# Kernel optimization log

Measured on AMD Instinct MI355X. Metric: run time of the kernel, lower is better.

Reference implementation:

```python
import jax, jax.numpy as jnp
import numpy as np
from jax import lax

B, T, V, E, H, L = 128, 256, 50000, 300, 512, 96


def masked_lstm(x, mask, W, U, b):
    """Keras-semantics masked LSTM, return_sequences=True.
    x: [B,T,D], mask: [B,T] bool. Gate order i,f,c,o (Keras).
    Masked steps carry h,c forward (output at masked step = previous output)."""
    Hs = U.shape[0]
    # input-to-hidden done as one big GEMM outside the scan
    xg = jnp.einsum('btd,dg->btg', x, W) + b  # [B,T,4H]
    h0 = jnp.zeros((x.shape[0], Hs), x.dtype)
    c0 = jnp.zeros((x.shape[0], Hs), x.dtype)

    def step(carry, inp):
        h, c = carry
        g_x, m = inp  # [B,4H], [B]
        g = g_x + h @ U
        i = jax.nn.sigmoid(g[:, :Hs])
        f = jax.nn.sigmoid(g[:, Hs:2 * Hs])
        cand = jnp.tanh(g[:, 2 * Hs:3 * Hs])
        o = jax.nn.sigmoid(g[:, 3 * Hs:])
        c_new = f * c + i * cand
        h_new = o * jnp.tanh(c_new)
        m = m[:, None]
        h_new = jnp.where(m, h_new, h)
        c_new = jnp.where(m, c_new, c)
        return (h_new, c_new), h_new

    (_, _), hs = lax.scan(step, (h0, c0), (xg.transpose(1, 0, 2), mask.T))
    return hs.transpose(1, 0, 2)  # [B,T,H]


def setup_inputs() -> dict:
    key = jax.random.key(0)
    ks = jax.random.split(key, 11)
    word_ids = jax.random.randint(ks[0], (B, T), 0, V, dtype=jnp.int32)
    predicate_ids = jax.random.randint(ks[1], (B, T), 0, 2, dtype=jnp.int32)
    emb = jax.random.normal(ks[2], (V, E), jnp.float32) * 0.1
    W1 = jax.random.normal(ks[3], (E + 1, 4 * H), jnp.float32) * 0.05
    U1 = jax.random.normal(ks[4], (H, 4 * H), jnp.float32) * 0.05
    b1 = jnp.zeros((4 * H,), jnp.float32)
    W2 = jax.random.normal(ks[5], (H, 4 * H), jnp.float32) * 0.05
    U2 = jax.random.normal(ks[6], (H, 4 * H), jnp.float32) * 0.05
    b2 = jnp.zeros((4 * H,), jnp.float32)
    Wd = jax.random.normal(ks[7], (H, L), jnp.float32) * 0.05
    bd = jnp.zeros((L,), jnp.float32)
    return {"word_ids": word_ids, "predicate_ids": predicate_ids,
            "emb": emb, "W1": W1, "U1": U1, "b1": b1,
            "W2": W2, "U2": U2, "b2": b2, "Wd": Wd, "bd": bd,
            "training": 0}


def reference(word_ids, predicate_ids, emb, W1, U1, b1, W2, U2, b2, Wd, bd, training):
    # training=0 -> dropout disabled (keep_prob=1.0 anyway)
    mask = word_ids != 0  # mask_zero semantics of the Embedding layer
    x = emb[word_ids]  # [B,T,E]
    flag = predicate_ids.astype(x.dtype)[..., None]  # [B,T,1]
    x = jnp.concatenate([x, flag], axis=2)  # [B,T,E+1]
    h1 = masked_lstm(x, mask, W1, U1, b1)
    h2 = masked_lstm(h1, mask, W2, U2, b2)
    enc = h2.reshape(-1, U1.shape[0])  # [B*T, H]
    return jax.nn.softmax(enc @ Wd + bd, axis=-1)  # [B*T, L]
```

## Files before the change

kernel.cpp:

```cpp
#include <hip/hip_runtime.h>
#include <hip/hip_bf16.h>

#define T_SEQ 256
#define HID 512
#define G4 2048
#define ASTR 80

typedef __attribute__((ext_vector_type(8))) short short8;
typedef __attribute__((ext_vector_type(4))) float floatx4;
typedef __attribute__((ext_vector_type(4))) int intx4;

__device__ inline unsigned short f2bf(float f) {
  union { __hip_bfloat16 h; unsigned short u; } cv;
  cv.h = __float2bfloat16(f);
  return cv.u;
}
__device__ inline float bf2f(unsigned short u) {
  union { unsigned short u; __hip_bfloat16 h; } cv;
  cv.u = u;
  return __bfloat162float(cv.h);
}
__device__ inline float fsigmoid(float x) {
  return __builtin_amdgcn_rcpf(1.0f + __expf(-x));
}
__device__ inline float ftanh(float x) {
  float e = __expf(2.0f * x);
  return 1.0f - 2.0f * __builtin_amdgcn_rcpf(e + 1.0f);
}

__device__ __forceinline__ void bar_lgkm() {
  asm volatile("s_waitcnt lgkmcnt(0)\n\ts_barrier" ::: "memory");
}

__global__ __launch_bounds__(256) void transpose_bf16(const float* __restrict__ src,
                                                      unsigned short* __restrict__ dst,
                                                      int K, int N, int Kpad) {
  __shared__ float tile[32][33];
  int n0 = blockIdx.x * 32, k0 = blockIdx.y * 32;
  int tx = threadIdx.x & 31, ty = threadIdx.x >> 5;
#pragma unroll
  for (int i = 0; i < 32; i += 8) {
    int k = k0 + ty + i, n = n0 + tx;
    tile[ty + i][tx] = (k < K) ? src[(size_t)k * N + n] : 0.0f;
  }
  __syncthreads();
#pragma unroll
  for (int i = 0; i < 32; i += 8) {
    int n = n0 + ty + i, k = k0 + tx;
    dst[(size_t)n * Kpad + k] = f2bf(tile[tx][ty + i]);
  }
}

__global__ __launch_bounds__(256) void gemm_xg1(const float* __restrict__ emb,
                                                const int* __restrict__ wid,
                                                const int* __restrict__ pred,
                                                const unsigned short* __restrict__ Bt,
                                                unsigned short* __restrict__ C) {
  int m0 = blockIdx.x * 64;
  int tid = threadIdx.x, lane = tid & 63, w = tid >> 6;
  __shared__ __align__(16) short As[64][328];
  __shared__ __align__(16) short Bs[2][64][40];
  {
    int grow = tid >> 2, gpart = tid & 3;
    int wrow = wid[m0 + grow];
    float pflag = (float)pred[m0 + grow];
    const float* erow = emb + (size_t)wrow * 300;
#pragma unroll
    for (int i = 0; i < 10; i++) {
      int c0 = gpart * 80 + i * 8;
      float f[8];
      if (c0 + 8 <= 300) {
        float4 x0 = *(const float4*)(erow + c0);
        float4 x1 = *(const float4*)(erow + c0 + 4);
        f[0] = x0.x; f[1] = x0.y; f[2] = x0.z; f[3] = x0.w;
        f[4] = x1.x; f[5] = x1.y; f[6] = x1.z; f[7] = x1.w;
      } else {
#pragma unroll
        for (int j = 0; j < 8; j++) {
          int k = c0 + j;
          f[j] = (k < 300) ? erow[k] : ((k == 300) ? pflag : 0.0f);
        }
      }
      short8 v;
#pragma unroll
      for (int j = 0; j < 8; j++) v[j] = (short)f2bf(f[j]);
      *(short8*)&As[grow][c0] = v;
    }
  }
  int brow = tid >> 2, bpart = tid & 3;
  for (int n0 = 0; n0 < 2048; n0 += 64) {
    *(short8*)&Bs[0][brow][bpart * 8] =
        *(const short8*)(Bt + (size_t)(n0 + brow) * 320 + bpart * 8);
    bar_lgkm();
    floatx4 acc[4];
#pragma unroll
    for (int i = 0; i < 4; i++) acc[i] = (floatx4){0.f, 0.f, 0.f, 0.f};
#pragma unroll
    for (int ks = 0; ks < 10; ks++) {
      if (ks < 9)
        *(short8*)&Bs[(ks + 1) & 1][brow][bpart * 8] =
            *(const short8*)(Bt + (size_t)(n0 + brow) * 320 + (ks + 1) * 32 + bpart * 8);
      short8 afr = *(const short8*)&As[w * 16 + (lane & 15)][ks * 32 + (lane >> 4) * 8];
#pragma unroll
      for (int nc = 0; nc < 4; nc++) {
        short8 bfr = *(const short8*)&Bs[ks & 1][nc * 16 + (lane & 15)][(lane >> 4) * 8];
        acc[nc] = __builtin_amdgcn_mfma_f32_16x16x32_bf16(afr, bfr, acc[nc], 0, 0, 0);
      }
      bar_lgkm();
    }
#pragma unroll
    for (int nc = 0; nc < 4; nc++)
#pragma unroll
      for (int r = 0; r < 4; r++) {
        int rr = m0 + w * 16 + ((lane >> 4) << 2) + r;
        int cc = n0 + nc * 16 + (lane & 15);
        C[(size_t)rr * G4 + cc] = f2bf(acc[nc][r]);
      }
  }
}

__device__ __forceinline__ void stage_issue(const unsigned int* base, int c16,
                                            intx4 (&v)[8], unsigned done) {
#pragma unroll
  for (int i = 0; i < 8; i++) {
    if (!(done & (1u << i))) {
      const unsigned int* p = base + 8 * c16 + 128 * (i >> 1) + 4 * (i & 1);
      asm volatile("global_load_dwordx4 %0, %1, off sc0 sc1" : "=v"(v[i]) : "v"(p) : "memory");
    }
  }
}
__device__ __forceinline__ void stage_check(unsigned want, char* AhRow, int sw, int c16,
                                            intx4 (&v)[8], unsigned& done) {
  asm volatile("s_waitcnt vmcnt(0)" ::: "memory");
#pragma unroll
  for (int i = 0; i < 8; i++) {
    if (!(done & (1u << i))) {
      intx4 a = v[i];
      unsigned u0 = (unsigned)a.x, u1 = (unsigned)a.y, u2 = (unsigned)a.z, u3 = (unsigned)a.w;
      bool ok = ((u0 >> 16) == want) & ((u1 >> 16) == want) & ((u2 >> 16) == want) &
                ((u3 >> 16) == want);
      if (ok) {
        unsigned lo = (u0 & 0xffffu) | (u1 << 16);
        unsigned hi = (u2 & 0xffffu) | (u3 << 16);
        int s = c16 + 16 * (i >> 1);
        uint2 pp; pp.x = lo; pp.y = hi;
        *(uint2*)(AhRow + ((s * 16) ^ sw) + (i & 1) * 8) = pp;
        done |= (1u << i);
      }
    }
  }
}
__device__ __forceinline__ void stage_wait(const unsigned int* base, unsigned want,
                                           char* AhRow, int sw, int c16) {
  intx4 v[8];
  unsigned done = 0;
  stage_issue(base, c16, v, done);
  stage_check(want, AhRow, sw, c16, v, done);
  while (done != 0xFFu) {
    __builtin_amdgcn_s_sleep(1);
    stage_issue(base, c16, v, done);
    stage_check(want, AhRow, sw, c16, v, done);
  }
}

__global__ __launch_bounds__(256, 1) void lstm_merged(
    const unsigned short* __restrict__ xg1,
    const unsigned short* __restrict__ Ut1, const float* __restrict__ b1,
    const unsigned short* __restrict__ Wt2, const unsigned short* __restrict__ Ut2,
    const float* __restrict__ b2, const int* __restrict__ wid,
    unsigned int* ex, unsigned short* h2seq) {
  const int blk = blockIdx.x;
  const int bgrp = blk & 7, jblk = blk >> 3;
  const int b0 = bgrp * 16, j0 = jblk * 16;
  const int tid = threadIdx.x, lane = tid & 63, w = tid >> 6;

  __shared__ __align__(16) char AhA[16 * 1024];
  __shared__ __align__(16) char AhB[16 * 1024];
  __shared__ float g1s[4][16][16];
  __shared__ float g2s[4][16][16];
  __shared__ float cst1[16][16];
  __shared__ float cst2[16][16];
  __shared__ __align__(16) unsigned short xgt[4][16][16];

  const int row = tid >> 4, c16 = tid & 15;
  const int sw = (row & 7) << 4;
  char* AhRowA = AhA + row * 1024;
  char* AhRowB = AhB + row * 1024;
  const int ucol = w * 512 + j0 + (lane & 15);
  const int* widp = wid + (size_t)(b0 + row) * T_SEQ;

  short8 uf1[16], wf2[16], uf2[16];
  {
    const unsigned short* p1 = Ut1 + (size_t)ucol * 512 + ((lane >> 4) * 8);
    const unsigned short* p2 = Wt2 + (size_t)ucol * 512 + ((lane >> 4) * 8);
    const unsigned short* p3 = Ut2 + (size_t)ucol * 512 + ((lane >> 4) * 8);
#pragma unroll
    for (int kk = 0; kk < 16; kk++) {
      uf1[kk] = *(const short8*)(p1 + kk * 32);
      wf2[kk] = *(const short8*)(p2 + kk * 32);
      uf2[kk] = *(const short8*)(p3 + kk * 32);
    }
  }
  float b1v = b1[ucol], b2v = b2[ucol];
  cst1[row][c16] = 0.0f;
  cst2[row][c16] = 0.0f;
  {
    short8 z = {0, 0, 0, 0, 0, 0, 0, 0};
    for (int i = tid; i < 1024; i += 256) {
      *(short8*)(AhA + i * 16) = z;
      *(short8*)(AhB + i * 16) = z;
    }
  }
  __syncthreads();

  int xg_g = tid >> 6, xg_rw = (tid >> 2) & 15, xg_part = tid & 3;
  uint2 xpf = *(const uint2*)(xg1 + ((size_t)(b0 + xg_rw) * T_SEQ + 0) * G4 + xg_g * 512 + j0 +
                              xg_part * 4);
  int mcur = widp[0];
  int mprev = 0;

  const size_t SLOT = (size_t)2 * 128 * 512;
  const int frow = lane & 15, kbase = (lane >> 4) * 16, fsw = (frow & 7) << 4;

  for (int t = 0; t <= T_SEQ; t++) {
    if (t > 0) {
      const unsigned int* bA = ex + (size_t)((t - 1) & 1) * SLOT + (size_t)(b0 + row) * 512;
      stage_wait(bA, (unsigned)t, AhRowA, sw, c16);
    }
    if (t < T_SEQ) {
      *(uint2*)(&xgt[xg_g][xg_rw][xg_part * 4]) = xpf;
      if (t + 1 < T_SEQ)
        xpf = *(const uint2*)(xg1 + ((size_t)(b0 + xg_rw) * T_SEQ + (t + 1)) * G4 + xg_g * 512 +
                              j0 + xg_part * 4);
    }
    bar_lgkm();

    floatx4 a1x = (floatx4){0.f, 0.f, 0.f, 0.f};
    floatx4 a1y = (floatx4){0.f, 0.f, 0.f, 0.f};
#pragma unroll
    for (int kk = 0; kk < 16; kk += 2) {
      short8 a0 = *(const short8*)(AhA + frow * 1024 + ((kk * 64 + kbase) ^ fsw));
      short8 a1 = *(const short8*)(AhA + frow * 1024 + (((kk + 1) * 64 + kbase) ^ fsw));
      a1x = __builtin_amdgcn_mfma_f32_16x16x32_bf16(a0, uf1[kk], a1x, 0, 0, 0);
      a1y = __builtin_amdgcn_mfma_f32_16x16x32_bf16(a1, uf1[kk + 1], a1y, 0, 0, 0);
    }
    if (t < T_SEQ) {
#pragma unroll
      for (int r = 0; r < 4; r++) {
        int grow = ((lane >> 4) << 2) + r, gcol = lane & 15;
        g1s[w][grow][gcol] = a1x[r] + a1y[r] + b1v + bf2f(xgt[w][grow][gcol]);
      }
    }
    bar_lgkm();

    if (t < T_SEQ) {
      float gi = g1s[0][row][c16], gf = g1s[1][row][c16];
      float gc = g1s[2][row][c16], go = g1s[3][row][c16];
      float iv = fsigmoid(gi), fv = fsigmoid(gf), cd = ftanh(gc), ov = fsigmoid(go);
      float cold = cst1[row][c16];
      float cn = fv * cold + iv * cd;
      float hn = ov * ftanh(cn);
      if (mcur == 0) {
        cn = cold;
        hn = bf2f(*(const unsigned short*)(AhRowA + (((j0 + c16) * 2) ^ sw)));
      }
      cst1[row][c16] = cn;
      unsigned v1 = (((unsigned)(t + 1)) << 16) | f2bf(hn);
      unsigned int* d1 = ex + (size_t)(t & 1) * SLOT + (size_t)(b0 + row) * 512 + j0 + c16;
      asm volatile("global_store_dword %0, %1, off sc0 sc1" ::"v"(d1), "v"(v1) : "memory");
    }
    if (t == 0) {
      unsigned v2 = 1u << 16;
      unsigned int* d2 =
          ex + (size_t)128 * 512 + (size_t)(b0 + row) * 512 + j0 + c16;
      asm volatile("global_store_dword %0, %1, off sc0 sc1" ::"v"(d2), "v"(v2) : "memory");
    }

    if (t > 0) {
      intx4 pend[8];
      unsigned doneB = 0;
      const unsigned int* bB = ex + (size_t)((t - 1) & 1) * SLOT + (size_t)128 * 512 +
                               (size_t)(b0 + row) * 512;
      stage_issue(bB, c16, pend, doneB);

      floatx4 a2x = (floatx4){0.f, 0.f, 0.f, 0.f};
      floatx4 a2y = (floatx4){0.f, 0.f, 0.f, 0.f};
#pragma unroll
      for (int kk = 0; kk < 16; kk += 2) {
        short8 a0 = *(const short8*)(AhA + frow * 1024 + ((kk * 64 + kbase) ^ fsw));
        short8 a1 = *(const short8*)(AhA + frow * 1024 + (((kk + 1) * 64 + kbase) ^ fsw));
        a2x = __builtin_amdgcn_mfma_f32_16x16x32_bf16(a0, wf2[kk], a2x, 0, 0, 0);
        a2y = __builtin_amdgcn_mfma_f32_16x16x32_bf16(a1, wf2[kk + 1], a2y, 0, 0, 0);
      }

      stage_check((unsigned)t, AhRowB, sw, c16, pend, doneB);
      while (doneB != 0xFFu) {
        __builtin_amdgcn_s_sleep(1);
        stage_issue(bB, c16, pend, doneB);
        stage_check((unsigned)t, AhRowB, sw, c16, pend, doneB);
      }
      bar_lgkm();

#pragma unroll
      for (int kk = 0; kk < 16; kk += 2) {
        short8 a0 = *(const short8*)(AhB + frow * 1024 + ((kk * 64 + kbase) ^ fsw));
        short8 a1 = *(const short8*)(AhB + frow * 1024 + (((kk + 1) * 64 + kbase) ^ fsw));
        a2x = __builtin_amdgcn_mfma_f32_16x16x32_bf16(a0, uf2[kk], a2x, 0, 0, 0);
        a2y = __builtin_amdgcn_mfma_f32_16x16x32_bf16(a1, uf2[kk + 1], a2y, 0, 0, 0);
      }
#pragma unroll
      for (int r = 0; r < 4; r++) {
        int grow = ((lane >> 4) << 2) + r, gcol = lane & 15;
        g2s[w][grow][gcol] = a2x[r] + a2y[r] + b2v;
      }
      bar_lgkm();

      {
        float gi = g2s[0][row][c16], gf = g2s[1][row][c16];
        float gc = g2s[2][row][c16], go = g2s[3][row][c16];
        float iv = fsigmoid(gi), fv = fsigmoid(gf), cd = ftanh(gc), ov = fsigmoid(go);
        float cold = cst2[row][c16];
        float cn = fv * cold + iv * cd;
        float hn = ov * ftanh(cn);
        if (mprev == 0) {
          cn = cold;
          hn = bf2f(*(const unsigned short*)(AhRowB + (((j0 + c16) * 2) ^ sw)));
        }
        cst2[row][c16] = cn;
        unsigned short hb = f2bf(hn);
        if (t < T_SEQ) {
          unsigned v2 = (((unsigned)(t + 1)) << 16) | hb;
          unsigned int* d2 = ex + (size_t)(t & 1) * SLOT + (size_t)128 * 512 +
                             (size_t)(b0 + row) * 512 + j0 + c16;
          asm volatile("global_store_dword %0, %1, off sc0 sc1" ::"v"(d2), "v"(v2) : "memory");
        }
        h2seq[((size_t)(b0 + row) * T_SEQ + (t - 1)) * HID + j0 + c16] = hb;
      }
      bar_lgkm();
    } else {
      bar_lgkm();
    }
    mprev = mcur;
    mcur = (t + 1 < T_SEQ) ? widp[t + 1] : 0;
  }
}

__global__ __launch_bounds__(256) void dense_softmax(const unsigned short* __restrict__ h2,
                                                     const unsigned short* __restrict__ Wdt,
                                                     const float* __restrict__ bd,
                                                     float* __restrict__ out) {
  int m0 = blockIdx.x * 64;
  int tid = threadIdx.x, lane = tid & 63, w = tid >> 6;
  __shared__ __align__(16) char As[64 * ASTR];
  __shared__ __align__(16) char Bs[96 * ASTR];
  floatx4 acc[6];
#pragma unroll
  for (int i = 0; i < 6; i++) acc[i] = (floatx4){0.f, 0.f, 0.f, 0.f};
  for (int k0 = 0; k0 < 512; k0 += 32) {
    {
      int row = tid >> 2, part = tid & 3;
      short8 v = *(const short8*)(h2 + (size_t)(m0 + row) * 512 + k0 + part * 8);
      *(short8*)(As + row * ASTR + part * 16) = v;
    }
    for (int u = tid; u < 96 * 4; u += 256) {
      int col = u >> 2, part = u & 3;
      short8 v = *(const short8*)(Wdt + (size_t)col * 512 + k0 + part * 8);
      *(short8*)(Bs + col * ASTR + part * 16) = v;
    }
    __syncthreads();
    int arow = w * 16 + (lane & 15);
    short8 a = *(const short8*)(As + arow * ASTR + (lane >> 4) * 16);
#pragma unroll
    for (int nc = 0; nc < 6; nc++) {
      int bcol = nc * 16 + (lane & 15);
      short8 b = *(const short8*)(Bs + bcol * ASTR + (lane >> 4) * 16);
      acc[nc] = __builtin_amdgcn_mfma_f32_16x16x32_bf16(a, b, acc[nc], 0, 0, 0);
    }
    __syncthreads();
  }
  float bv[6];
#pragma unroll
  for (int nc = 0; nc < 6; nc++) bv[nc] = bd[nc * 16 + (lane & 15)];
#pragma unroll
  for (int r = 0; r < 4; r++) {
    float v[6];
    float mx = -1e30f;
#pragma unroll
    for (int nc = 0; nc < 6; nc++) {
      v[nc] = acc[nc][r] + bv[nc];
      mx = fmaxf(mx, v[nc]);
    }
#pragma unroll
    for (int d = 1; d < 16; d <<= 1) mx = fmaxf(mx, __shfl_xor(mx, d));
    float s = 0.f;
#pragma unroll
    for (int nc = 0; nc < 6; nc++) {
      v[nc] = __expf(v[nc] - mx);
      s += v[nc];
    }
#pragma unroll
    for (int d = 1; d < 16; d <<= 1) s += __shfl_xor(s, d);
    float inv = 1.0f / s;
    int rr = m0 + w * 16 + ((lane >> 4) << 2) + r;
#pragma unroll
    for (int nc = 0; nc < 6; nc++) out[(size_t)rr * 96 + nc * 16 + (lane & 15)] = v[nc] * inv;
  }
}

extern "C" void kernel_launch(void* const* d_in, const int* in_sizes, int n_in,
                              void* d_out, int out_size, void* d_ws, size_t ws_size,
                              hipStream_t stream) {
  (void)in_sizes; (void)n_in; (void)out_size; (void)ws_size;
  const int* word_ids = (const int*)d_in[0];
  const int* pred = (const int*)d_in[1];
  const float* emb = (const float*)d_in[2];
  const float* W1 = (const float*)d_in[3];
  const float* U1 = (const float*)d_in[4];
  const float* b1 = (const float*)d_in[5];
  const float* W2 = (const float*)d_in[6];
  const float* U2 = (const float*)d_in[7];
  const float* b2 = (const float*)d_in[8];
  const float* Wd = (const float*)d_in[9];
  const float* bd = (const float*)d_in[10];
  float* out = (float*)d_out;

  const size_t EXBYTES = (size_t)2 * 2 * 128 * 512 * 4;

  char* p = (char*)d_ws;
  unsigned short* xg = (unsigned short*)p;   p += (size_t)32768 * 2048 * 2;
  unsigned short* h2s = (unsigned short*)p;  p += (size_t)32768 * 512 * 2;
  unsigned int* ex = (unsigned int*)p;       p += EXBYTES;
  unsigned short* Ut1 = (unsigned short*)p;  p += (size_t)2048 * 512 * 2;
  unsigned short* Ut2 = (unsigned short*)p;  p += (size_t)2048 * 512 * 2;
  unsigned short* Wt1 = (unsigned short*)p;  p += (size_t)2048 * 320 * 2;
  unsigned short* Wt2 = (unsigned short*)p;  p += (size_t)2048 * 512 * 2;
  unsigned short* Wdt = (unsigned short*)p;  p += (size_t)96 * 512 * 2;

  hipMemsetAsync(ex, 0, EXBYTES, stream);

  hipLaunchKernelGGL(transpose_bf16, dim3(64, 16), dim3(256), 0, stream, U1, Ut1, 512, 2048, 512);
  hipLaunchKernelGGL(transpose_bf16, dim3(64, 16), dim3(256), 0, stream, U2, Ut2, 512, 2048, 512);
  hipLaunchKernelGGL(transpose_bf16, dim3(64, 10), dim3(256), 0, stream, W1, Wt1, 301, 2048, 320);
  hipLaunchKernelGGL(transpose_bf16, dim3(64, 16), dim3(256), 0, stream, W2, Wt2, 512, 2048, 512);
  hipLaunchKernelGGL(transpose_bf16, dim3(3, 16), dim3(256), 0, stream, Wd, Wdt, 512, 96, 512);

  hipLaunchKernelGGL(gemm_xg1, dim3(512), dim3(256), 0, stream,
                     emb, word_ids, pred, Wt1, xg);
  hipLaunchKernelGGL(lstm_merged, dim3(256), dim3(256), 0, stream,
                     xg, Ut1, b1, Wt2, Ut2, b2, word_ids, ex, h2s);
  hipLaunchKernelGGL(dense_softmax, dim3(512), dim3(256), 0, stream, h2s, Wdt, bd, out);
}
```

Before: 1.515 ms.

## Prefetch next-step layer-1 exchange loads early, move U2 weights to LDS

The spin-wait loads for the next timestep's layer-1 hidden-state exchange are now issued at the end of the current iteration, so their latency overlaps the loop tail instead of sitting on the critical path. The layer-2 recurrent weights move from registers into a swizzled LDS buffer to cut register pressure, and the kernel pins waves_per_eu to 1. Bias and xg gate inputs are held per thread in registers and added during the elementwise phase, which removes the xgt shared staging array and merges the two gate buffers into one. The cost is extra LDS reads per MFMA in the layer-2 recurrence and a check against stale prefetched data that may need to re-poll.

```diff
diff --git a/kernel.cpp b/kernel.cpp
--- a/kernel.cpp
+++ b/kernel.cpp
@@ -119,18 +119,18 @@
   }
 }
 
-__device__ __forceinline__ void stage_issue(const unsigned int* base, int c16,
-                                            intx4 (&v)[8], unsigned done) {
+__device__ __forceinline__ void stg_issue(const unsigned int* rowbase, int c16,
+                                          intx4 (&v)[8], unsigned done) {
 #pragma unroll
   for (int i = 0; i < 8; i++) {
     if (!(done & (1u << i))) {
-      const unsigned int* p = base + 8 * c16 + 128 * (i >> 1) + 4 * (i & 1);
+      const unsigned int* p = rowbase + 8 * c16 + 128 * (i >> 1) + 4 * (i & 1);
       asm volatile("global_load_dwordx4 %0, %1, off sc0 sc1" : "=v"(v[i]) : "v"(p) : "memory");
     }
   }
 }
-__device__ __forceinline__ void stage_check(unsigned want, char* AhRow, int sw, int c16,
-                                            intx4 (&v)[8], unsigned& done) {
+__device__ __forceinline__ void stg_check(unsigned want, char* AhRow, int sw, int c16,
+                                          intx4 (&v)[8], unsigned& done) {
   asm volatile("s_waitcnt vmcnt(0)" ::: "memory");
 #pragma unroll
   for (int i = 0; i < 8; i++) {
@@ -140,30 +140,29 @@
       bool ok = ((u0 >> 16) == want) & ((u1 >> 16) == want) & ((u2 >> 16) == want) &
                 ((u3 >> 16) == want);
       if (ok) {
-        unsigned lo = (u0 & 0xffffu) | (u1 << 16);
-        unsigned hi = (u2 & 0xffffu) | (u3 << 16);
+        uint2 pp;
+        pp.x = (u0 & 0xffffu) | (u1 << 16);
+        pp.y = (u2 & 0xffffu) | (u3 << 16);
         int s = c16 + 16 * (i >> 1);
-        uint2 pp; pp.x = lo; pp.y = hi;
         *(uint2*)(AhRow + ((s * 16) ^ sw) + (i & 1) * 8) = pp;
         done |= (1u << i);
       }
     }
   }
 }
-__device__ __forceinline__ void stage_wait(const unsigned int* base, unsigned want,
-                                           char* AhRow, int sw, int c16) {
-  intx4 v[8];
-  unsigned done = 0;
-  stage_issue(base, c16, v, done);
-  stage_check(want, AhRow, sw, c16, v, done);
+__device__ __forceinline__ void stg_finish(const unsigned int* rowbase, unsigned want,
+                                           char* AhRow, int sw, int c16,
+                                           intx4 (&v)[8], unsigned& done) {
+  stg_check(want, AhRow, sw, c16, v, done);
   while (done != 0xFFu) {
     __builtin_amdgcn_s_sleep(1);
-    stage_issue(base, c16, v, done);
-    stage_check(want, AhRow, sw, c16, v, done);
-  }
-}
-
-__global__ __launch_bounds__(256, 1) void lstm_merged(
+    stg_issue(rowbase, c16, v, done);
+    stg_check(want, AhRow, sw, c16, v, done);
+  }
+}
+
+__global__ __launch_bounds__(256, 1) __attribute__((amdgpu_waves_per_eu(1, 1)))
+void lstm_merged(
     const unsigned short* __restrict__ xg1,
     const unsigned short* __restrict__ Ut1, const float* __restrict__ b1,
     const unsigned short* __restrict__ Wt2, const unsigned short* __restrict__ Ut2,
@@ -176,11 +175,10 @@
 
   __shared__ __align__(16) char AhA[16 * 1024];
   __shared__ __align__(16) char AhB[16 * 1024];
-  __shared__ float g1s[4][16][16];
-  __shared__ float g2s[4][16][16];
+  __shared__ __align__(16) char U2L[64 * 1024];
+  __shared__ float gds[4][16][16];
   __shared__ float cst1[16][16];
   __shared__ float cst2[16][16];
-  __shared__ __align__(16) unsigned short xgt[4][16][16];
 
   const int row = tid >> 4, c16 = tid & 15;
   const int sw = (row & 7) << 4;
@@ -189,19 +187,27 @@
   const int ucol = w * 512 + j0 + (lane & 15);
   const int* widp = wid + (size_t)(b0 + row) * T_SEQ;
 
-  short8 uf1[16], wf2[16], uf2[16];
+  short8 uf1[16], wf2[16];
   {
     const unsigned short* p1 = Ut1 + (size_t)ucol * 512 + ((lane >> 4) * 8);
     const unsigned short* p2 = Wt2 + (size_t)ucol * 512 + ((lane >> 4) * 8);
-    const unsigned short* p3 = Ut2 + (size_t)ucol * 512 + ((lane >> 4) * 8);
 #pragma unroll
     for (int kk = 0; kk < 16; kk++) {
       uf1[kk] = *(const short8*)(p1 + kk * 32);
       wf2[kk] = *(const short8*)(p2 + kk * 32);
-      uf2[kk] = *(const short8*)(p3 + kk * 32);
-    }
-  }
-  float b1v = b1[ucol], b2v = b2[ucol];
+    }
+  }
+  for (int i = tid; i < 4096; i += 256) {
+    int r = i >> 6, seg = i & 63;
+    short8 v = *(const short8*)(Ut2 + (size_t)((r >> 4) * 512 + j0 + (r & 15)) * 512 + seg * 8);
+    *(short8*)(U2L + r * 1024 + ((seg * 16) ^ ((r & 7) << 4))) = v;
+  }
+  float b1v[4], b2v[4];
+#pragma unroll
+  for (int g = 0; g < 4; g++) {
+    b1v[g] = b1[g * 512 + j0 + c16];
+    b2v[g] = b2[g * 512 + j0 + c16];
+  }
   cst1[row][c16] = 0.0f;
   cst2[row][c16] = 0.0f;
   {
@@ -213,25 +219,25 @@
   }
   __syncthreads();
 
-  int xg_g = tid >> 6, xg_rw = (tid >> 2) & 15, xg_part = tid & 3;
-  uint2 xpf = *(const uint2*)(xg1 + ((size_t)(b0 + xg_rw) * T_SEQ + 0) * G4 + xg_g * 512 + j0 +
-                              xg_part * 4);
+  const unsigned short* xgrow = xg1 + (size_t)(b0 + row) * T_SEQ * G4 + j0 + c16;
+  unsigned short xc[4], xn[4];
+#pragma unroll
+  for (int g = 0; g < 4; g++) { xc[g] = xgrow[g * 512]; xn[g] = 0; }
   int mcur = widp[0];
   int mprev = 0;
 
   const size_t SLOT = (size_t)2 * 128 * 512;
   const int frow = lane & 15, kbase = (lane >> 4) * 16, fsw = (frow & 7) << 4;
+  const int urow = w * 16 + (lane & 15);
+  const int usw = (urow & 7) << 4;
+
+  intx4 pendA[8], pendB[8];
+  unsigned doneA = 0xFFu;
 
   for (int t = 0; t <= T_SEQ; t++) {
     if (t > 0) {
       const unsigned int* bA = ex + (size_t)((t - 1) & 1) * SLOT + (size_t)(b0 + row) * 512;
-      stage_wait(bA, (unsigned)t, AhRowA, sw, c16);
-    }
-    if (t < T_SEQ) {
-      *(uint2*)(&xgt[xg_g][xg_rw][xg_part * 4]) = xpf;
-      if (t + 1 < T_SEQ)
-        xpf = *(const uint2*)(xg1 + ((size_t)(b0 + xg_rw) * T_SEQ + (t + 1)) * G4 + xg_g * 512 +
-                              j0 + xg_part * 4);
+      stg_finish(bA, (unsigned)t, AhRowA, sw, c16, pendA, doneA);
     }
     bar_lgkm();
 
@@ -240,22 +246,22 @@
 #pragma unroll
     for (int kk = 0; kk < 16; kk += 2) {
       short8 a0 = *(const short8*)(AhA + frow * 1024 + ((kk * 64 + kbase) ^ fsw));
-      short8 a1 = *(const short8*)(AhA + frow * 1024 + (((kk + 1) * 64 + kbase) ^ fsw));
+      short8 a1f = *(const short8*)(AhA + frow * 1024 + (((kk + 1) * 64 + kbase) ^ fsw));
       a1x = __builtin_amdgcn_mfma_f32_16x16x32_bf16(a0, uf1[kk], a1x, 0, 0, 0);
-      a1y = __builtin_amdgcn_mfma_f32_16x16x32_bf16(a1, uf1[kk + 1], a1y, 0, 0, 0);
+      a1y = __builtin_amdgcn_mfma_f32_16x16x32_bf16(a1f, uf1[kk + 1], a1y, 0, 0, 0);
     }
     if (t < T_SEQ) {
 #pragma unroll
-      for (int r = 0; r < 4; r++) {
-        int grow = ((lane >> 4) << 2) + r, gcol = lane & 15;
-        g1s[w][grow][gcol] = a1x[r] + a1y[r] + b1v + bf2f(xgt[w][grow][gcol]);
-      }
+      for (int r = 0; r < 4; r++)
+        gds[w][((lane >> 4) << 2) + r][lane & 15] = a1x[r] + a1y[r];
     }
     bar_lgkm();
 
     if (t < T_SEQ) {
-      float gi = g1s[0][row][c16], gf = g1s[1][row][c16];
-      float gc = g1s[2][row][c16], go = g1s[3][row][c16];
+      float gi = gds[0][row][c16] + b1v[0] + bf2f(xc[0]);
+      float gf = gds[1][row][c16] + b1v[1] + bf2f(xc[1]);
+      float gc = gds[2][row][c16] + b1v[2] + bf2f(xc[2]);
+      float go = gds[3][row][c16] + b1v[3] + bf2f(xc[3]);
       float iv = fsigmoid(gi), fv = fsigmoid(gf), cd = ftanh(gc), ov = fsigmoid(go);
       float cold = cst1[row][c16];
       float cn = fv * cold + iv * cd;
@@ -271,53 +277,53 @@
     }
     if (t == 0) {
       unsigned v2 = 1u << 16;
-      unsigned int* d2 =
-          ex + (size_t)128 * 512 + (size_t)(b0 + row) * 512 + j0 + c16;
+      unsigned int* d2 = ex + (size_t)128 * 512 + (size_t)(b0 + row) * 512 + j0 + c16;
       asm volatile("global_store_dword %0, %1, off sc0 sc1" ::"v"(d2), "v"(v2) : "memory");
     }
+    if (t + 1 < T_SEQ) {
+      const unsigned short* xr = xgrow + (size_t)(t + 1) * G4;
+#pragma unroll
+      for (int g = 0; g < 4; g++) xn[g] = xr[g * 512];
+    }
 
     if (t > 0) {
-      intx4 pend[8];
       unsigned doneB = 0;
       const unsigned int* bB = ex + (size_t)((t - 1) & 1) * SLOT + (size_t)128 * 512 +
                                (size_t)(b0 + row) * 512;
-      stage_issue(bB, c16, pend, doneB);
+      stg_issue(bB, c16, pendB, doneB);
 
       floatx4 a2x = (floatx4){0.f, 0.f, 0.f, 0.f};
       floatx4 a2y = (floatx4){0.f, 0.f, 0.f, 0.f};
 #pragma unroll
       for (int kk = 0; kk < 16; kk += 2) {
         short8 a0 = *(const short8*)(AhA + frow * 1024 + ((kk * 64 + kbase) ^ fsw));
-        short8 a1 = *(const short8*)(AhA + frow * 1024 + (((kk + 1) * 64 + kbase) ^ fsw));
+        short8 a1f = *(const short8*)(AhA + frow * 1024 + (((kk + 1) * 64 + kbase) ^ fsw));
         a2x = __builtin_amdgcn_mfma_f32_16x16x32_bf16(a0, wf2[kk], a2x, 0, 0, 0);
-        a2y = __builtin_amdgcn_mfma_f32_16x16x32_bf16(a1, wf2[kk + 1], a2y, 0, 0, 0);
-      }
-
-      stage_check((unsigned)t, AhRowB, sw, c16, pend, doneB);
-      while (doneB != 0xFFu) {
-        __builtin_amdgcn_s_sleep(1);
-        stage_issue(bB, c16, pend, doneB);
-        stage_check((unsigned)t, AhRowB, sw, c16, pend, doneB);
-      }
+        a2y = __builtin_amdgcn_mfma_f32_16x16x32_bf16(a1f, wf2[kk + 1], a2y, 0, 0, 0);
+      }
+
+      stg_finish(bB, (unsigned)t, AhRowB, sw, c16, pendB, doneB);
       bar_lgkm();
 
 #pragma unroll
       for (int kk = 0; kk < 16; kk += 2) {
         short8 a0 = *(const short8*)(AhB + frow * 1024 + ((kk * 64 + kbase) ^ fsw));
-        short8 a1 = *(const short8*)(AhB + frow * 1024 + (((kk + 1) * 64 + kbase) ^ fsw));
-        a2x = __builtin_amdgcn_mfma_f32_16x16x32_bf16(a0, uf2[kk], a2x, 0, 0, 0);
-        a2y = __builtin_amdgcn_mfma_f32_16x16x32_bf16(a1, uf2[kk + 1], a2y, 0, 0, 0);
-      }
-#pragma unroll
-      for (int r = 0; r < 4; r++) {
-        int grow = ((lane >> 4) << 2) + r, gcol = lane & 15;
-        g2s[w][grow][gcol] = a2x[r] + a2y[r] + b2v;
-      }
+        short8 u0 = *(const short8*)(U2L + urow * 1024 + ((kk * 64 + kbase) ^ usw));
+        short8 a1f = *(const short8*)(AhB + frow * 1024 + (((kk + 1) * 64 + kbase) ^ fsw));
+        short8 u1 = *(const short8*)(U2L + urow * 1024 + (((kk + 1) * 64 + kbase) ^ usw));
+        a2x = __builtin_amdgcn_mfma_f32_16x16x32_bf16(a0, u0, a2x, 0, 0, 0);
+        a2y = __builtin_amdgcn_mfma_f32_16x16x32_bf16(a1f, u1, a2y, 0, 0, 0);
+      }
+#pragma unroll
+      for (int r = 0; r < 4; r++)
+        gds[w][((lane >> 4) << 2) + r][lane & 15] = a2x[r] + a2y[r];
       bar_lgkm();
 
       {
-        float gi = g2s[0][row][c16], gf = g2s[1][row][c16];
-        float gc = g2s[2][row][c16], go = g2s[3][row][c16];
+        float gi = gds[0][row][c16] + b2v[0];
+        float gf = gds[1][row][c16] + b2v[1];
+        float gc = gds[2][row][c16] + b2v[2];
+        float go = gds[3][row][c16] + b2v[3];
         float iv = fsigmoid(gi), fv = fsigmoid(gf), cd = ftanh(gc), ov = fsigmoid(go);
         float cold = cst2[row][c16];
         float cn = fv * cold + iv * cd;
@@ -340,8 +346,16 @@
     } else {
       bar_lgkm();
     }
+
+    if (t < T_SEQ) {
+      const unsigned int* bA2 = ex + (size_t)(t & 1) * SLOT + (size_t)(b0 + row) * 512;
+      doneA = 0;
+      stg_issue(bA2, c16, pendA, doneA);
+    }
     mprev = mcur;
     mcur = (t + 1 < T_SEQ) ? widp[t + 1] : 0;
+#pragma unroll
+    for (int g = 0; g < 4; g++) xc[g] = xn[g];
   }
 }
 
```

After: 1.430 ms. -5.6%, faster.
